# Kernel tuning notes

Hardware: AMD Instinct MI355X
Metric: run time of the kernel (lower is better)

Reference implementation:

```python
import jax, jax.numpy as jnp
import numpy as np

N, E, IN, H, C, ED = 100000, 1600000, 128, 4, 32, 16
HC = H * C
NEG_SLOPE = 0.2
EPS = 1e-5


def setup_inputs() -> dict:
    key = jax.random.key(0)
    ks = jax.random.split(key, 12)
    x = jax.random.normal(ks[0], (N, IN), jnp.float32)
    edge_index = jax.random.randint(ks[1], (2, E), 0, N, dtype=jnp.int32)
    edge_attr = jax.random.normal(ks[2], (E, ED), jnp.float32)
    s_in = 1.0 / np.sqrt(IN)
    s_ed = 1.0 / np.sqrt(ED)
    s_c = 1.0 / np.sqrt(C)
    Wl = jax.random.normal(ks[3], (IN, HC), jnp.float32) * s_in
    bl = jnp.zeros((HC,), jnp.float32)
    Wr = jax.random.normal(ks[4], (IN, HC), jnp.float32) * s_in
    br = jnp.zeros((HC,), jnp.float32)
    We = jax.random.normal(ks[5], (ED, HC), jnp.float32) * s_ed
    att = jax.random.normal(ks[6], (H, C), jnp.float32) * s_c
    bias = jnp.zeros((HC,), jnp.float32)
    ln_weight = jnp.ones((HC,), jnp.float32)
    ln_bias = jnp.zeros((HC,), jnp.float32)
    return {"x": x, "edge_index": edge_index, "edge_attr": edge_attr,
            "Wl": Wl, "bl": bl, "Wr": Wr, "br": br, "We": We,
            "att": att, "bias": bias, "ln_weight": ln_weight, "ln_bias": ln_bias}


def gatv2_block(x, src, dst, edge_attr, Wl, bl, Wr, br, We, att, bias, ln_weight, ln_bias):
    n = x.shape[0]
    xl = (x @ Wl + bl).reshape(n, H, C)  # source-side transform
    xr = (x @ Wr + br).reshape(n, H, C)  # target-side transform
    # add_self_loops with fill_value='mean': self-loop edge_attr = mean of
    # incoming edge_attr per node (0 for isolated nodes)
    ea_sum = jax.ops.segment_sum(edge_attr, dst, num_segments=n)
    cnt = jax.ops.segment_sum(jnp.ones((edge_attr.shape[0],), edge_attr.dtype), dst, num_segments=n)
    self_attr = ea_sum / jnp.maximum(cnt, 1.0)[:, None]
    loop = jnp.arange(n, dtype=src.dtype)
    src_a = jnp.concatenate([src, loop])
    dst_a = jnp.concatenate([dst, loop])
    ea_a = jnp.concatenate([edge_attr, self_attr], axis=0)
    e_emb = (ea_a @ We).reshape(-1, H, C)
    # GATv2 attention: a^T LeakyReLU(xl_j + xr_i + e)
    m = xl[src_a] + xr[dst_a] + e_emb            # [Etot, H, C]
    m = jax.nn.leaky_relu(m, NEG_SLOPE)
    alpha = jnp.einsum('ehc,hc->eh', m, att)     # [Etot, H]
    amax = jax.ops.segment_max(alpha, dst_a, num_segments=n)
    alpha = jnp.exp(alpha - amax[dst_a])
    denom = jax.ops.segment_sum(alpha, dst_a, num_segments=n)
    alpha = alpha / denom[dst_a]
    out = jax.ops.segment_sum(xl[src_a] * alpha[:, :, None], dst_a, num_segments=n)
    h = out.reshape(n, HC) + bias
    # residual (in_dim == H*C so no projection), PyG graph-mode LayerNorm
    z = x + h
    mu = jnp.mean(z)
    var = jnp.mean((z - mu) ** 2)
    z = (z - mu) / jnp.sqrt(var + EPS)
    z = z * ln_weight + ln_bias
    return jax.nn.relu(z)  # dropout = identity in eval


def reference(x, edge_index, edge_attr, Wl, bl, Wr, br, We, att, bias, ln_weight, ln_bias):
    src, dst = edge_index[0], edge_index[1]
    return gatv2_block(x, src, dst, edge_attr, Wl, bl, Wr, br, We, att, bias, ln_weight, ln_bias)
```

## Files before the change

### kernel.cpp

```cpp
#include <hip/hip_runtime.h>
#include <hip/hip_bf16.h>

static constexpr float NEG_SLOPE = 0.2f;
static constexpr float LN_EPS = 1e-5f;

typedef float v2f __attribute__((ext_vector_type(2)));
typedef __attribute__((ext_vector_type(8))) short bf16x8;
typedef __attribute__((ext_vector_type(4))) float f32x4;

__device__ __forceinline__ unsigned f2b(float f) {
  unsigned u = __float_as_uint(f);
  return (u + 0x7fffu + ((u >> 16) & 1u)) >> 16;
}
__device__ __forceinline__ v2f b2f2(ushort2 u) {
  v2f r;
  r.x = __uint_as_float((unsigned)u.x << 16);
  r.y = __uint_as_float((unsigned)u.y << 16);
  return r;
}
__device__ __forceinline__ float sbl(unsigned w) {
  return __uint_as_float(w << 16);
}
__device__ __forceinline__ float sbh(unsigned w) {
  return __uint_as_float(w & 0xFFFF0000u);
}

__device__ __forceinline__ float head_sum16(float x) {
  float t;
  t = __int_as_float(__builtin_amdgcn_update_dpp(
      0, __float_as_int(x), 0xB1, 0xF, 0xF, true));
  x += t;
  t = __int_as_float(__builtin_amdgcn_update_dpp(
      0, __float_as_int(x), 0x4E, 0xF, 0xF, true));
  x += t;
  t = __int_as_float(__builtin_amdgcn_update_dpp(
      0, __float_as_int(x), 0x124, 0xF, 0xF, true));
  x += t;
  t = __int_as_float(__builtin_amdgcn_update_dpp(
      0, __float_as_int(x), 0x128, 0xF, 0xF, true));
  x += t;
  return x;
}

__global__ __launch_bounds__(256) void k_packB(
    const float* __restrict__ Wl, const float* __restrict__ Wr,
    const float* __restrict__ bl, const float* __restrict__ br,
    ushort* __restrict__ Bpack, float* __restrict__ bcat)
{
  int tid = blockIdx.x * 256 + threadIdx.x;
  int l = tid & 63, s = (tid >> 6) & 3, t = tid >> 8;
  int col = t * 16 + (l & 15);
  int kb = s * 32 + (l >> 4) * 8;
  const float* __restrict__ W = (col < 128) ? Wl : Wr;
  int c = col & 127;
  unsigned p[4];
#pragma unroll
  for (int i = 0; i < 4; ++i) {
    unsigned lo = f2b(W[(size_t)(kb + 2 * i) * 128 + c]);
    unsigned hi = f2b(W[(size_t)(kb + 2 * i + 1) * 128 + c]);
    p[i] = lo | (hi << 16);
  }
  *(uint4*)(Bpack + (size_t)tid * 8) = make_uint4(p[0], p[1], p[2], p[3]);
  if (tid < 256) bcat[tid] = (tid < 128) ? bl[tid] : br[tid - 128];
}

__global__ __launch_bounds__(256) void k_gemm_mfma(
    const float* __restrict__ x, const ushort* __restrict__ Bpack,
    const float* __restrict__ bcat, ushort* __restrict__ xl,
    float* __restrict__ outz, int n)
{
  const int lane = threadIdx.x & 63;
  const int w = threadIdx.x >> 6;
  const int row0 = blockIdx.x * 64 + w * 16;
  const int rowA = min(row0 + (lane & 15), n - 1);
  const int kgrp = lane >> 4;

  f32x4 acc[16];
#pragma unroll
  for (int t = 0; t < 16; ++t) acc[t] = (f32x4){0.f, 0.f, 0.f, 0.f};

#pragma unroll
  for (int s = 0; s < 4; ++s) {
    const float4* ap =
        (const float4*)(x + (size_t)rowA * 128 + s * 32 + kgrp * 8);
    float4 a0 = ap[0], a1 = ap[1];
    bf16x8 a;
    a[0] = (short)f2b(a0.x); a[1] = (short)f2b(a0.y);
    a[2] = (short)f2b(a0.z); a[3] = (short)f2b(a0.w);
    a[4] = (short)f2b(a1.x); a[5] = (short)f2b(a1.y);
    a[6] = (short)f2b(a1.z); a[7] = (short)f2b(a1.w);
#pragma unroll
    for (int t = 0; t < 16; ++t) {
      bf16x8 b =
          *(const bf16x8*)(Bpack + (((size_t)t * 4 + s) * 64 + lane) * 8);
      acc[t] = __builtin_amdgcn_mfma_f32_16x16x32_bf16(a, b, acc[t], 0, 0, 0);
    }
  }

  const int colg = lane & 15;
  const int rbase = row0 + (lane >> 4) * 4;
#pragma unroll
  for (int t = 0; t < 16; ++t) {
    const int col = t * 16 + colg;
    const float bia = bcat[col];
    if (col < 128) {
#pragma unroll
      for (int r = 0; r < 4; ++r) {
        const int R = rbase + r;
        if (R < n) xl[(size_t)R * 128 + col] = (ushort)f2b(acc[t][r] + bia);
      }
    } else {
      const int c = col - 128;
#pragma unroll
      for (int r = 0; r < 4; ++r) {
        const int R = rbase + r;
        if (R < n) outz[(size_t)R * 128 + c] = acc[t][r] + bia;
      }
    }
  }
}

__global__ __launch_bounds__(256) void k_count(const int* __restrict__ dst,
                                               int* __restrict__ deg, int E)
{
  int e = blockIdx.x * 256 + threadIdx.x;
  if (e < E) atomicAdd(&deg[dst[e]], 1);
}

__global__ __launch_bounds__(256) void k_scan1(const int* __restrict__ deg,
                                               int* __restrict__ bsum, int n)
{
  int i = blockIdx.x * 256 + threadIdx.x;
  int v = (i < n) ? deg[i] : 0;
#pragma unroll
  for (int o = 32; o > 0; o >>= 1) v += __shfl_down(v, o);
  __shared__ int ls[4];
  if ((threadIdx.x & 63) == 0) ls[threadIdx.x >> 6] = v;
  __syncthreads();
  if (threadIdx.x == 0) bsum[blockIdx.x] = ls[0] + ls[1] + ls[2] + ls[3];
}

__global__ __launch_bounds__(512) void k_scan2(int* __restrict__ bsum, int nb)
{
  __shared__ int s[512];
  int t = threadIdx.x;
  int v = (t < nb) ? bsum[t] : 0;
  s[t] = v;
  __syncthreads();
  for (int o = 1; o < 512; o <<= 1) {
    int u = (t >= o) ? s[t - o] : 0;
    __syncthreads();
    s[t] += u;
    __syncthreads();
  }
  if (t < nb) bsum[t] = s[t] - v;
}

__global__ __launch_bounds__(256) void k_scan3(const int* __restrict__ deg,
                                               const int* __restrict__ bsum,
                                               int* __restrict__ offs, int n)
{
  __shared__ int s[256];
  int b = blockIdx.x, t = threadIdx.x, i = b * 256 + t;
  int v = (i < n) ? deg[i] : 0;
  s[t] = v;
  __syncthreads();
  for (int o = 1; o < 256; o <<= 1) {
    int u = (t >= o) ? s[t - o] : 0;
    __syncthreads();
    s[t] += u;
    __syncthreads();
  }
  if (i < n) offs[i] = bsum[b] + s[t] - v;
}

__global__ __launch_bounds__(256) void k_fill(
    const int* __restrict__ src, const int* __restrict__ dst,
    const int* __restrict__ offs, int* __restrict__ cursor,
    const float4* __restrict__ ea4, int* __restrict__ csr_src,
    ushort* __restrict__ csr_ea, int E)
{
  int e = blockIdx.x * 256 + threadIdx.x;
  if (e >= E) return;
  int d = dst[e];
  int pos = offs[d] + atomicAdd(&cursor[d], 1);
  csr_src[pos] = src[e];
  float4 r0 = ea4[(size_t)e * 4 + 0], r1 = ea4[(size_t)e * 4 + 1];
  float4 r2 = ea4[(size_t)e * 4 + 2], r3 = ea4[(size_t)e * 4 + 3];
  uint4* o4 = (uint4*)(csr_ea + (size_t)pos * 16);
  o4[0] = make_uint4(f2b(r0.x) | (f2b(r0.y) << 16), f2b(r0.z) | (f2b(r0.w) << 16),
                     f2b(r1.x) | (f2b(r1.y) << 16), f2b(r1.z) | (f2b(r1.w) << 16));
  o4[1] = make_uint4(f2b(r2.x) | (f2b(r2.y) << 16), f2b(r2.z) | (f2b(r2.w) << 16),
                     f2b(r3.x) | (f2b(r3.y) << 16), f2b(r3.z) | (f2b(r3.w) << 16));
}

__global__ __launch_bounds__(256) void k_fused(
    const int* __restrict__ csr_src, const ushort* __restrict__ csr_ea,
    const int* __restrict__ offs, const int* __restrict__ deg,
    const ushort* __restrict__ xl, const float* __restrict__ We,
    const float* __restrict__ att, const float* __restrict__ x,
    const float* __restrict__ bias, float* __restrict__ outz,
    double* __restrict__ red, int N)
{
  const int lane = threadIdx.x & 63;
  const int gw =
      __builtin_amdgcn_readfirstlane(blockIdx.x * 4 + (threadIdx.x >> 6));
  const int nw = gridDim.x * 4;
  const v2f* __restrict__ We2 = (const v2f*)We;
  const v2f* __restrict__ X2 = (const v2f*)x;
  v2f* __restrict__ Z2 = (v2f*)outz;

  v2f we[16];
#pragma unroll
  for (int k = 0; k < 16; ++k) we[k] = We2[k * 64 + lane];
  const v2f a2 = ((const v2f*)att)[lane];
  const v2f b2 = ((const v2f*)bias)[lane];

  float sred = 0.f, s2red = 0.f;

  for (int node = gw; node < N; node += nw) {
    const int beg = offs[node];
    const int len = deg[node];
    const v2f xrv = Z2[(size_t)node * 64 + lane];
    const v2f xvSelf =
        b2f2(*(const ushort2*)(xl + (size_t)node * 128 + 2 * lane));

    float dA = 0.f, dB = 0.f;
    v2f aA = {0.f, 0.f}, aB = {0.f, 0.f};
    v2f embsum = {0.f, 0.f};

    auto edgeU = [&](v2f xv, uint4 lo, uint4 hi, float& den, v2f& acc) {
      v2f emb = sbl(lo.x) * we[0];
      emb += sbh(lo.x) * we[1];
      emb += sbl(lo.y) * we[2];
      emb += sbh(lo.y) * we[3];
      emb += sbl(lo.z) * we[4];
      emb += sbh(lo.z) * we[5];
      emb += sbl(lo.w) * we[6];
      emb += sbh(lo.w) * we[7];
      emb += sbl(hi.x) * we[8];
      emb += sbh(hi.x) * we[9];
      emb += sbl(hi.y) * we[10];
      emb += sbh(hi.y) * we[11];
      emb += sbl(hi.z) * we[12];
      emb += sbh(hi.z) * we[13];
      emb += sbl(hi.w) * we[14];
      emb += sbh(hi.w) * we[15];
      embsum += emb;
      v2f mm = xv + xrv + emb;
      v2f ml;
      ml.x = fmaxf(mm.x, NEG_SLOPE * mm.x);
      ml.y = fmaxf(mm.y, NEG_SLOPE * mm.y);
      const float part = head_sum16(fmaf(ml.y, a2.y, ml.x * a2.x));
      const float p = __expf(part);
      den += p;
      acc += xv * p;
    };

    const int nB = len >> 1;
    const int nA = len - nB;
    const int bB = beg + nA;

    uint4 eAlo = {0, 0, 0, 0}, eAhi = {0, 0, 0, 0};
    uint4 eBlo = {0, 0, 0, 0}, eBhi = {0, 0, 0, 0};
    v2f xvA = {0.f, 0.f}, xvB = {0.f, 0.f};
    int sA1 = 0, sB1 = 0;

    if (len > 0) {
      const uint4* pa = (const uint4*)(csr_ea + (size_t)beg * 16);
      eAlo = pa[0];
      eAhi = pa[1];
      const int sA0 = csr_src[beg];
      xvA = b2f2(*(const ushort2*)(xl + (size_t)sA0 * 128 + 2 * lane));
      sA1 = csr_src[beg + 1];
    }
    if (nB > 0) {
      const uint4* pb = (const uint4*)(csr_ea + (size_t)bB * 16);
      eBlo = pb[0];
      eBhi = pb[1];
      const int sB0 = csr_src[bB];
      xvB = b2f2(*(const ushort2*)(xl + (size_t)sB0 * 128 + 2 * lane));
      sB1 = csr_src[bB + 1];
    }

    for (int i = 0; i < nB; ++i) {
      const uint4* pa = (const uint4*)(csr_ea + (size_t)(beg + i + 1) * 16);
      const uint4* pb = (const uint4*)(csr_ea + (size_t)(bB + i + 1) * 16);
      const uint4 nAlo = pa[0], nAhi = pa[1];
      const uint4 nBlo = pb[0], nBhi = pb[1];
      const v2f xvA1 =
          b2f2(*(const ushort2*)(xl + (size_t)sA1 * 128 + 2 * lane));
      const v2f xvB1 =
          b2f2(*(const ushort2*)(xl + (size_t)sB1 * 128 + 2 * lane));
      const int sA2 = csr_src[beg + i + 2];
      const int sB2 = csr_src[bB + i + 2];
      edgeU(xvA, eAlo, eAhi, dA, aA);
      edgeU(xvB, eBlo, eBhi, dB, aB);
      eAlo = nAlo; eAhi = nAhi; eBlo = nBlo; eBhi = nBhi;
      xvA = xvA1; xvB = xvB1;
      sA1 = sA2; sB1 = sB2;
    }
    if (nA > nB) {
      edgeU(xvA, eAlo, eAhi, dA, aA);
    }

    {
      const float inv = (len > 0) ? 1.f / (float)len : 0.f;
      const v2f embS = embsum * inv;
      v2f mm = xvSelf + xrv + embS;
      v2f ml;
      ml.x = fmaxf(mm.x, NEG_SLOPE * mm.x);
      ml.y = fmaxf(mm.y, NEG_SLOPE * mm.y);
      const float part = head_sum16(fmaf(ml.y, a2.y, ml.x * a2.x));
      const float p = __expf(part);
      dA += p;
      aA += xvSelf * p;
    }

    const float den = dA + dB;
    const float invden = 1.f / den;
    const float o0 = (aA.x + aB.x) * invden;
    const float o1 = (aA.y + aB.y) * invden;

    const v2f xvn = X2[(size_t)node * 64 + lane];
    const float v0 = xvn.x + o0 + b2.x;
    const float v1 = xvn.y + o1 + b2.y;
    Z2[(size_t)node * 64 + lane] = (v2f){v0, v1};
    sred += v0 + v1;
    s2red += v0 * v0 + v1 * v1;
  }

#pragma unroll
  for (int o = 32; o > 0; o >>= 1) {
    sred += __shfl_down(sred, o);
    s2red += __shfl_down(s2red, o);
  }
  __shared__ double ls[4], ls2[4];
  const int w = threadIdx.x >> 6;
  if ((threadIdx.x & 63) == 0) {
    ls[w] = (double)sred;
    ls2[w] = (double)s2red;
  }
  __syncthreads();
  if (threadIdx.x == 0) {
    unsafeAtomicAdd(red, ls[0] + ls[1] + ls[2] + ls[3]);
    unsafeAtomicAdd(red + 1, ls2[0] + ls2[1] + ls2[2] + ls2[3]);
  }
}

__global__ __launch_bounds__(256) void k_final(
    float* __restrict__ z, const double* __restrict__ red,
    const float* __restrict__ lnw, const float* __restrict__ lnb, int M4)
{
  int i = blockIdx.x * 256 + threadIdx.x;
  if (i >= M4) return;
  const double invM = 1.0 / ((double)M4 * 4.0);
  const double mu = red[0] * invM;
  const double var = red[1] * invM - mu * mu;
  const float sc = rsqrtf((float)var + LN_EPS);
  const float muf = (float)mu;
  const float4* W4 = (const float4*)lnw;
  const float4* L4 = (const float4*)lnb;
  float4* Z4 = (float4*)z;
  float4 zv = Z4[i], wv = W4[i & 31], lv = L4[i & 31];
  float4 o;
  o.x = fmaxf((zv.x - muf) * sc * wv.x + lv.x, 0.f);
  o.y = fmaxf((zv.y - muf) * sc * wv.y + lv.y, 0.f);
  o.z = fmaxf((zv.z - muf) * sc * wv.z + lv.z, 0.f);
  o.w = fmaxf((zv.w - muf) * sc * wv.w + lv.w, 0.f);
  Z4[i] = o;
}

extern "C" void kernel_launch(void* const* d_in, const int* in_sizes, int n_in,
                              void* d_out, int out_size, void* d_ws,
                              size_t ws_size, hipStream_t stream)
{
  const float* x = (const float*)d_in[0];
  const int* ei = (const int*)d_in[1];
  const float* edge_attr = (const float*)d_in[2];
  const float* Wl = (const float*)d_in[3];
  const float* bl = (const float*)d_in[4];
  const float* Wr = (const float*)d_in[5];
  const float* br = (const float*)d_in[6];
  const float* We = (const float*)d_in[7];
  const float* att = (const float*)d_in[8];
  const float* bias = (const float*)d_in[9];
  const float* lnw = (const float*)d_in[10];
  const float* lnb = (const float*)d_in[11];
  float* out = (float*)d_out;

  const int N = in_sizes[0] / 128;
  const int E = in_sizes[1] / 2;
  const int M = N * 128;
  const int* srcp = ei;
  const int* dstp = ei + E;
  const int nb = (N + 255) / 256;

  ushort* xl = (ushort*)d_ws;
  int* deg = (int*)(xl + (size_t)M);
  int* cursor = deg + N;
  int* offs = cursor + N;
  int* bsum = offs + N;
  int* csr_src = bsum + ((nb + 7) & ~7);
  ushort* csr_ea =
      (ushort*)((((size_t)(csr_src + E + 8)) + 63) & ~(size_t)63);
  double* red = (double*)(
      (((size_t)(csr_ea + (size_t)E * 16 + 16)) + 127) & ~(size_t)127);
  ushort* Bpack = (ushort*)(red + 8);
  float* bcat = (float*)(Bpack + 4096 * 8);

  hipMemsetAsync(deg, 0, (size_t)N * 8, stream);
  hipMemsetAsync(csr_src + E, 0, 32, stream);
  hipMemsetAsync(red, 0, 16, stream);

  k_packB<<<16, 256, 0, stream>>>(Wl, Wr, bl, br, Bpack, bcat);
  k_gemm_mfma<<<(N + 63) / 64, 256, 0, stream>>>(x, Bpack, bcat, xl, out, N);
  k_count<<<(E + 255) / 256, 256, 0, stream>>>(dstp, deg, E);
  k_scan1<<<nb, 256, 0, stream>>>(deg, bsum, N);
  k_scan2<<<1, 512, 0, stream>>>(bsum, nb);
  k_scan3<<<nb, 256, 0, stream>>>(deg, bsum, offs, N);
  k_fill<<<(E + 255) / 256, 256, 0, stream>>>(srcp, dstp, offs, cursor,
                                              (const float4*)edge_attr,
                                              csr_src, csr_ea, E);
  k_fused<<<2048, 256, 0, stream>>>(csr_src, csr_ea, offs, deg, xl, We, att,
                                    x, bias, out, red, N);
  k_final<<<(M / 4 + 255) / 256, 256, 0, stream>>>(out, red, lnw, lnb, M / 4);
}
```

Measured before the change: 498.5 us.

## Deepen edge-attr prefetch to two edges, split emb FMA chain, fold memsets into packB

In the fused edge loop, edge attributes are now prefetched two iterations ahead instead of one, so more loads are in flight to hide memory latency. The serial 16-term embedding accumulation is split into four independent chains to shorten the dependency path. Two small memsets are moved into the k_packB kernel to cut API launch overhead, and the padding after csr_ea is enlarged to cover the deeper prefetch. The cost is higher register pressure from the extra buffered uint4 values, plus slightly different floating-point summation order.

Measured after the change: 499.6 us. About the same (+0.2%).

```diff
diff --git a/kernel.cpp b/kernel.cpp
--- a/kernel.cpp
+++ b/kernel.cpp
@@ -45,7 +45,8 @@
 __global__ __launch_bounds__(256) void k_packB(
     const float* __restrict__ Wl, const float* __restrict__ Wr,
     const float* __restrict__ bl, const float* __restrict__ br,
-    ushort* __restrict__ Bpack, float* __restrict__ bcat)
+    ushort* __restrict__ Bpack, float* __restrict__ bcat,
+    int* __restrict__ src_pad, double* __restrict__ red)
 {
   int tid = blockIdx.x * 256 + threadIdx.x;
   int l = tid & 63, s = (tid >> 6) & 3, t = tid >> 8;
@@ -62,6 +63,8 @@
   }
   *(uint4*)(Bpack + (size_t)tid * 8) = make_uint4(p[0], p[1], p[2], p[3]);
   if (tid < 256) bcat[tid] = (tid < 128) ? bl[tid] : br[tid - 128];
+  if (tid < 8) src_pad[tid] = 0;
+  if (tid < 2) red[tid] = 0.0;
 }
 
 __global__ __launch_bounds__(256) void k_gemm_mfma(
@@ -230,22 +233,23 @@
     v2f embsum = {0.f, 0.f};
 
     auto edgeU = [&](v2f xv, uint4 lo, uint4 hi, float& den, v2f& acc) {
-      v2f emb = sbl(lo.x) * we[0];
-      emb += sbh(lo.x) * we[1];
-      emb += sbl(lo.y) * we[2];
-      emb += sbh(lo.y) * we[3];
-      emb += sbl(lo.z) * we[4];
-      emb += sbh(lo.z) * we[5];
-      emb += sbl(lo.w) * we[6];
-      emb += sbh(lo.w) * we[7];
-      emb += sbl(hi.x) * we[8];
-      emb += sbh(hi.x) * we[9];
-      emb += sbl(hi.y) * we[10];
-      emb += sbh(hi.y) * we[11];
-      emb += sbl(hi.z) * we[12];
-      emb += sbh(hi.z) * we[13];
-      emb += sbl(hi.w) * we[14];
-      emb += sbh(hi.w) * we[15];
+      v2f e0 = sbl(lo.x) * we[0];
+      v2f e1 = sbh(lo.x) * we[1];
+      v2f e2 = sbl(lo.y) * we[2];
+      v2f e3 = sbh(lo.y) * we[3];
+      e0 += sbl(lo.z) * we[4];
+      e1 += sbh(lo.z) * we[5];
+      e2 += sbl(lo.w) * we[6];
+      e3 += sbh(lo.w) * we[7];
+      e0 += sbl(hi.x) * we[8];
+      e1 += sbh(hi.x) * we[9];
+      e2 += sbl(hi.y) * we[10];
+      e3 += sbh(hi.y) * we[11];
+      e0 += sbl(hi.z) * we[12];
+      e1 += sbh(hi.z) * we[13];
+      e2 += sbl(hi.w) * we[14];
+      e3 += sbh(hi.w) * we[15];
+      const v2f emb = (e0 + e1) + (e2 + e3);
       embsum += emb;
       v2f mm = xv + xrv + emb;
       v2f ml;
@@ -262,7 +266,9 @@
     const int bB = beg + nA;
 
     uint4 eAlo = {0, 0, 0, 0}, eAhi = {0, 0, 0, 0};
+    uint4 eA1lo = {0, 0, 0, 0}, eA1hi = {0, 0, 0, 0};
     uint4 eBlo = {0, 0, 0, 0}, eBhi = {0, 0, 0, 0};
+    uint4 eB1lo = {0, 0, 0, 0}, eB1hi = {0, 0, 0, 0};
     v2f xvA = {0.f, 0.f}, xvB = {0.f, 0.f};
     int sA1 = 0, sB1 = 0;
 
@@ -270,6 +276,9 @@
       const uint4* pa = (const uint4*)(csr_ea + (size_t)beg * 16);
       eAlo = pa[0];
       eAhi = pa[1];
+      const uint4* pa1 = (const uint4*)(csr_ea + (size_t)(beg + 1) * 16);
+      eA1lo = pa1[0];
+      eA1hi = pa1[1];
       const int sA0 = csr_src[beg];
       xvA = b2f2(*(const ushort2*)(xl + (size_t)sA0 * 128 + 2 * lane));
       sA1 = csr_src[beg + 1];
@@ -278,16 +287,19 @@
       const uint4* pb = (const uint4*)(csr_ea + (size_t)bB * 16);
       eBlo = pb[0];
       eBhi = pb[1];
+      const uint4* pb1 = (const uint4*)(csr_ea + (size_t)(bB + 1) * 16);
+      eB1lo = pb1[0];
+      eB1hi = pb1[1];
       const int sB0 = csr_src[bB];
       xvB = b2f2(*(const ushort2*)(xl + (size_t)sB0 * 128 + 2 * lane));
       sB1 = csr_src[bB + 1];
     }
 
     for (int i = 0; i < nB; ++i) {
-      const uint4* pa = (const uint4*)(csr_ea + (size_t)(beg + i + 1) * 16);
-      const uint4* pb = (const uint4*)(csr_ea + (size_t)(bB + i + 1) * 16);
-      const uint4 nAlo = pa[0], nAhi = pa[1];
-      const uint4 nBlo = pb[0], nBhi = pb[1];
+      const uint4* pa2 = (const uint4*)(csr_ea + (size_t)(beg + i + 2) * 16);
+      const uint4* pb2 = (const uint4*)(csr_ea + (size_t)(bB + i + 2) * 16);
+      const uint4 eA2lo = pa2[0], eA2hi = pa2[1];
+      const uint4 eB2lo = pb2[0], eB2hi = pb2[1];
       const v2f xvA1 =
           b2f2(*(const ushort2*)(xl + (size_t)sA1 * 128 + 2 * lane));
       const v2f xvB1 =
@@ -296,7 +308,8 @@
       const int sB2 = csr_src[bB + i + 2];
       edgeU(xvA, eAlo, eAhi, dA, aA);
       edgeU(xvB, eBlo, eBhi, dB, aB);
-      eAlo = nAlo; eAhi = nAhi; eBlo = nBlo; eBhi = nBhi;
+      eAlo = eA1lo; eAhi = eA1hi; eA1lo = eA2lo; eA1hi = eA2hi;
+      eBlo = eB1lo; eBhi = eB1hi; eB1lo = eB2lo; eB1hi = eB2hi;
       xvA = xvA1; xvB = xvB1;
       sA1 = sA2; sB1 = sB2;
     }
@@ -405,15 +418,14 @@
   ushort* csr_ea =
       (ushort*)((((size_t)(csr_src + E + 8)) + 63) & ~(size_t)63);
   double* red = (double*)(
-      (((size_t)(csr_ea + (size_t)E * 16 + 16)) + 127) & ~(size_t)127);
+      (((size_t)(csr_ea + (size_t)E * 16 + 64)) + 127) & ~(size_t)127);
   ushort* Bpack = (ushort*)(red + 8);
   float* bcat = (float*)(Bpack + 4096 * 8);
 
   hipMemsetAsync(deg, 0, (size_t)N * 8, stream);
-  hipMemsetAsync(csr_src + E, 0, 32, stream);
-  hipMemsetAsync(red, 0, 16, stream);
-
-  k_packB<<<16, 256, 0, stream>>>(Wl, Wr, bl, br, Bpack, bcat);
+
+  k_packB<<<16, 256, 0, stream>>>(Wl, Wr, bl, br, Bpack, bcat, csr_src + E,
+                                  red);
   k_gemm_mfma<<<(N + 63) / 64, 256, 0, stream>>>(x, Bpack, bcat, xl, out, N);
   k_count<<<(E + 255) / 256, 256, 0, stream>>>(dstp, deg, E);
   k_scan1<<<nb, 256, 0, stream>>>(deg, bsum, N);
```

## Store xl in fp32, fuse degree count into GEMM, fold memsets into packB

Applied to the files above, without the earlier changes.

Switches the xl intermediate from bf16 to fp32, which doubles its storage and the bytes of every per-edge gather in the fused kernel but removes the bf16 pack/unpack steps. The per-edge degree atomic count moves into the tail of the GEMM kernel as a grid-stride loop, and the small memsets for the CSR padding and reduction accumulators move into the packB kernel. Together these drop two memsets and one kernel launch, at the cost of heavier gather traffic in the main aggregation loop.

After: 491.7 us. No clear change (-1.4%).

```diff
diff --git a/kernel.cpp b/kernel.cpp
--- a/kernel.cpp
+++ b/kernel.cpp
@@ -11,12 +11,6 @@
 __device__ __forceinline__ unsigned f2b(float f) {
   unsigned u = __float_as_uint(f);
   return (u + 0x7fffu + ((u >> 16) & 1u)) >> 16;
-}
-__device__ __forceinline__ v2f b2f2(ushort2 u) {
-  v2f r;
-  r.x = __uint_as_float((unsigned)u.x << 16);
-  r.y = __uint_as_float((unsigned)u.y << 16);
-  return r;
 }
 __device__ __forceinline__ float sbl(unsigned w) {
   return __uint_as_float(w << 16);
@@ -45,7 +39,8 @@
 __global__ __launch_bounds__(256) void k_packB(
     const float* __restrict__ Wl, const float* __restrict__ Wr,
     const float* __restrict__ bl, const float* __restrict__ br,
-    ushort* __restrict__ Bpack, float* __restrict__ bcat)
+    ushort* __restrict__ Bpack, float* __restrict__ bcat,
+    int* __restrict__ src_pad, double* __restrict__ red)
 {
   int tid = blockIdx.x * 256 + threadIdx.x;
   int l = tid & 63, s = (tid >> 6) & 3, t = tid >> 8;
@@ -62,12 +57,15 @@
   }
   *(uint4*)(Bpack + (size_t)tid * 8) = make_uint4(p[0], p[1], p[2], p[3]);
   if (tid < 256) bcat[tid] = (tid < 128) ? bl[tid] : br[tid - 128];
+  if (tid < 8) src_pad[tid] = 0;
+  if (tid < 2) red[tid] = 0.0;
 }
 
 __global__ __launch_bounds__(256) void k_gemm_mfma(
     const float* __restrict__ x, const ushort* __restrict__ Bpack,
-    const float* __restrict__ bcat, ushort* __restrict__ xl,
-    float* __restrict__ outz, int n)
+    const float* __restrict__ bcat, float* __restrict__ xl,
+    float* __restrict__ outz, int n, const int* __restrict__ dst,
+    int* __restrict__ deg, int E)
 {
   const int lane = threadIdx.x & 63;
   const int w = threadIdx.x >> 6;
@@ -103,28 +101,17 @@
   for (int t = 0; t < 16; ++t) {
     const int col = t * 16 + colg;
     const float bia = bcat[col];
-    if (col < 128) {
-#pragma unroll
-      for (int r = 0; r < 4; ++r) {
-        const int R = rbase + r;
-        if (R < n) xl[(size_t)R * 128 + col] = (ushort)f2b(acc[t][r] + bia);
-      }
-    } else {
-      const int c = col - 128;
-#pragma unroll
-      for (int r = 0; r < 4; ++r) {
-        const int R = rbase + r;
-        if (R < n) outz[(size_t)R * 128 + c] = acc[t][r] + bia;
-      }
-    }
-  }
-}
-
-__global__ __launch_bounds__(256) void k_count(const int* __restrict__ dst,
-                                               int* __restrict__ deg, int E)
-{
-  int e = blockIdx.x * 256 + threadIdx.x;
-  if (e < E) atomicAdd(&deg[dst[e]], 1);
+    float* __restrict__ outp = (col < 128) ? xl : outz;
+    const int c = col & 127;
+#pragma unroll
+    for (int r = 0; r < 4; ++r) {
+      const int R = rbase + r;
+      if (R < n) outp[(size_t)R * 128 + c] = acc[t][r] + bia;
+    }
+  }
+
+  for (int e = blockIdx.x * 256 + threadIdx.x; e < E; e += gridDim.x * 256)
+    atomicAdd(&deg[dst[e]], 1);
 }
 
 __global__ __launch_bounds__(256) void k_scan1(const int* __restrict__ deg,
@@ -197,7 +184,7 @@
 __global__ __launch_bounds__(256) void k_fused(
     const int* __restrict__ csr_src, const ushort* __restrict__ csr_ea,
     const int* __restrict__ offs, const int* __restrict__ deg,
-    const ushort* __restrict__ xl, const float* __restrict__ We,
+    const float* __restrict__ xl, const float* __restrict__ We,
     const float* __restrict__ att, const float* __restrict__ x,
     const float* __restrict__ bias, float* __restrict__ outz,
     double* __restrict__ red, int N)
@@ -207,6 +194,7 @@
       __builtin_amdgcn_readfirstlane(blockIdx.x * 4 + (threadIdx.x >> 6));
   const int nw = gridDim.x * 4;
   const v2f* __restrict__ We2 = (const v2f*)We;
+  const v2f* __restrict__ Xl2 = (const v2f*)xl;
   const v2f* __restrict__ X2 = (const v2f*)x;
   v2f* __restrict__ Z2 = (v2f*)outz;
 
@@ -222,8 +210,7 @@
     const int beg = offs[node];
     const int len = deg[node];
     const v2f xrv = Z2[(size_t)node * 64 + lane];
-    const v2f xvSelf =
-        b2f2(*(const ushort2*)(xl + (size_t)node * 128 + 2 * lane));
+    const v2f xvSelf = Xl2[(size_t)node * 64 + lane];
 
     float dA = 0.f, dB = 0.f;
     v2f aA = {0.f, 0.f}, aB = {0.f, 0.f};
@@ -271,7 +258,7 @@
       eAlo = pa[0];
       eAhi = pa[1];
       const int sA0 = csr_src[beg];
-      xvA = b2f2(*(const ushort2*)(xl + (size_t)sA0 * 128 + 2 * lane));
+      xvA = Xl2[(size_t)sA0 * 64 + lane];
       sA1 = csr_src[beg + 1];
     }
     if (nB > 0) {
@@ -279,7 +266,7 @@
       eBlo = pb[0];
       eBhi = pb[1];
       const int sB0 = csr_src[bB];
-      xvB = b2f2(*(const ushort2*)(xl + (size_t)sB0 * 128 + 2 * lane));
+      xvB = Xl2[(size_t)sB0 * 64 + lane];
       sB1 = csr_src[bB + 1];
     }
 
@@ -288,10 +275,8 @@
       const uint4* pb = (const uint4*)(csr_ea + (size_t)(bB + i + 1) * 16);
       const uint4 nAlo = pa[0], nAhi = pa[1];
       const uint4 nBlo = pb[0], nBhi = pb[1];
-      const v2f xvA1 =
-          b2f2(*(const ushort2*)(xl + (size_t)sA1 * 128 + 2 * lane));
-      const v2f xvB1 =
-          b2f2(*(const ushort2*)(xl + (size_t)sB1 * 128 + 2 * lane));
+      const v2f xvA1 = Xl2[(size_t)sA1 * 64 + lane];
+      const v2f xvB1 = Xl2[(size_t)sB1 * 64 + lane];
       const int sA2 = csr_src[beg + i + 2];
       const int sB2 = csr_src[bB + i + 2];
       edgeU(xvA, eAlo, eAhi, dA, aA);
@@ -396,7 +381,7 @@
   const int* dstp = ei + E;
   const int nb = (N + 255) / 256;
 
-  ushort* xl = (ushort*)d_ws;
+  float* xl = (float*)d_ws;
   int* deg = (int*)(xl + (size_t)M);
   int* cursor = deg + N;
   int* offs = cursor + N;
@@ -405,17 +390,16 @@
   ushort* csr_ea =
       (ushort*)((((size_t)(csr_src + E + 8)) + 63) & ~(size_t)63);
   double* red = (double*)(
-      (((size_t)(csr_ea + (size_t)E * 16 + 16)) + 127) & ~(size_t)127);
+      (((size_t)(csr_ea + (size_t)E * 16 + 64)) + 127) & ~(size_t)127);
   ushort* Bpack = (ushort*)(red + 8);
   float* bcat = (float*)(Bpack + 4096 * 8);
 
   hipMemsetAsync(deg, 0, (size_t)N * 8, stream);
-  hipMemsetAsync(csr_src + E, 0, 32, stream);
-  hipMemsetAsync(red, 0, 16, stream);
-
-  k_packB<<<16, 256, 0, stream>>>(Wl, Wr, bl, br, Bpack, bcat);
-  k_gemm_mfma<<<(N + 63) / 64, 256, 0, stream>>>(x, Bpack, bcat, xl, out, N);
-  k_count<<<(E + 255) / 256, 256, 0, stream>>>(dstp, deg, E);
+
+  k_packB<<<16, 256, 0, stream>>>(Wl, Wr, bl, br, Bpack, bcat, csr_src + E,
+                                  red);
+  k_gemm_mfma<<<(N + 63) / 64, 256, 0, stream>>>(x, Bpack, bcat, xl, out, N,
+                                                 dstp, deg, E);
   k_scan1<<<nb, 256, 0, stream>>>(deg, bsum, N);
   k_scan2<<<1, 512, 0, stream>>>(bsum, nb);
   k_scan3<<<nb, 256, 0, stream>>>(deg, bsum, offs, N);
```

## Fuse memsets and degree count into existing kernels, replace three-pass scan with atomic allocation

Applied to the files above, without the earlier changes.

Moves the zeroing of degree/cursor arrays, padding and reduction buffers into the weight-packing kernel, and folds the per-edge degree count into the tail of the GEMM kernel. It also replaces the three-kernel prefix scan with a single kernel in which each block scans locally and reserves its base offset through an atomic counter. CSR segments are then no longer laid out in node order, which relies on consumers using offs/deg rather than contiguity. The aim is fewer launches and memsets, at the cost of nondeterministic segment placement and extra work added to the GEMM.

Measured after the change: 485.2 us, median of 2. 1.03x faster.

```diff
diff --git a/kernel.cpp b/kernel.cpp
--- a/kernel.cpp
+++ b/kernel.cpp
@@ -45,7 +45,9 @@
 __global__ __launch_bounds__(256) void k_packB(
     const float* __restrict__ Wl, const float* __restrict__ Wr,
     const float* __restrict__ bl, const float* __restrict__ br,
-    ushort* __restrict__ Bpack, float* __restrict__ bcat)
+    ushort* __restrict__ Bpack, float* __restrict__ bcat,
+    int* __restrict__ degcur, int N2, int* __restrict__ tot,
+    int* __restrict__ src_pad, double* __restrict__ red)
 {
   int tid = blockIdx.x * 256 + threadIdx.x;
   int l = tid & 63, s = (tid >> 6) & 3, t = tid >> 8;
@@ -62,12 +64,17 @@
   }
   *(uint4*)(Bpack + (size_t)tid * 8) = make_uint4(p[0], p[1], p[2], p[3]);
   if (tid < 256) bcat[tid] = (tid < 128) ? bl[tid] : br[tid - 128];
+  if (tid < 8) src_pad[tid] = 0;
+  if (tid < 2) red[tid] = 0.0;
+  if (tid == 0) *tot = 0;
+  for (int i = tid; i < N2; i += 4096) degcur[i] = 0;
 }
 
 __global__ __launch_bounds__(256) void k_gemm_mfma(
     const float* __restrict__ x, const ushort* __restrict__ Bpack,
     const float* __restrict__ bcat, ushort* __restrict__ xl,
-    float* __restrict__ outz, int n)
+    float* __restrict__ outz, int n, const int* __restrict__ dst,
+    int* __restrict__ deg, int E)
 {
   const int lane = threadIdx.x & 63;
   const int w = threadIdx.x >> 6;
@@ -118,51 +125,19 @@
       }
     }
   }
-}
-
-__global__ __launch_bounds__(256) void k_count(const int* __restrict__ dst,
-                                               int* __restrict__ deg, int E)
-{
-  int e = blockIdx.x * 256 + threadIdx.x;
-  if (e < E) atomicAdd(&deg[dst[e]], 1);
-}
-
-__global__ __launch_bounds__(256) void k_scan1(const int* __restrict__ deg,
-                                               int* __restrict__ bsum, int n)
-{
-  int i = blockIdx.x * 256 + threadIdx.x;
-  int v = (i < n) ? deg[i] : 0;
-#pragma unroll
-  for (int o = 32; o > 0; o >>= 1) v += __shfl_down(v, o);
-  __shared__ int ls[4];
-  if ((threadIdx.x & 63) == 0) ls[threadIdx.x >> 6] = v;
-  __syncthreads();
-  if (threadIdx.x == 0) bsum[blockIdx.x] = ls[0] + ls[1] + ls[2] + ls[3];
-}
-
-__global__ __launch_bounds__(512) void k_scan2(int* __restrict__ bsum, int nb)
-{
-  __shared__ int s[512];
-  int t = threadIdx.x;
-  int v = (t < nb) ? bsum[t] : 0;
-  s[t] = v;
-  __syncthreads();
-  for (int o = 1; o < 512; o <<= 1) {
-    int u = (t >= o) ? s[t - o] : 0;
-    __syncthreads();
-    s[t] += u;
-    __syncthreads();
-  }
-  if (t < nb) bsum[t] = s[t] - v;
-}
-
-__global__ __launch_bounds__(256) void k_scan3(const int* __restrict__ deg,
-                                               const int* __restrict__ bsum,
-                                               int* __restrict__ offs, int n)
+
+  for (int e = blockIdx.x * 256 + threadIdx.x; e < E; e += gridDim.x * 256)
+    atomicAdd(&deg[dst[e]], 1);
+}
+
+__global__ __launch_bounds__(256) void k_allocscan(
+    const int* __restrict__ deg, int* __restrict__ offs, int* __restrict__ tot,
+    int n)
 {
   __shared__ int s[256];
-  int b = blockIdx.x, t = threadIdx.x, i = b * 256 + t;
-  int v = (i < n) ? deg[i] : 0;
+  __shared__ int base;
+  const int b = blockIdx.x, t = threadIdx.x, i = b * 256 + t;
+  const int v = (i < n) ? deg[i] : 0;
   s[t] = v;
   __syncthreads();
   for (int o = 1; o < 256; o <<= 1) {
@@ -171,7 +146,9 @@
     s[t] += u;
     __syncthreads();
   }
-  if (i < n) offs[i] = bsum[b] + s[t] - v;
+  if (t == 255) base = atomicAdd(tot, s[255]);
+  __syncthreads();
+  if (i < n) offs[i] = base + s[t] - v;
 }
 
 __global__ __launch_bounds__(256) void k_fill(
@@ -400,25 +377,20 @@
   int* deg = (int*)(xl + (size_t)M);
   int* cursor = deg + N;
   int* offs = cursor + N;
-  int* bsum = offs + N;
-  int* csr_src = bsum + ((nb + 7) & ~7);
+  int* tot = offs + N;
+  int* csr_src = tot + 8;
   ushort* csr_ea =
       (ushort*)((((size_t)(csr_src + E + 8)) + 63) & ~(size_t)63);
   double* red = (double*)(
-      (((size_t)(csr_ea + (size_t)E * 16 + 16)) + 127) & ~(size_t)127);
+      (((size_t)(csr_ea + (size_t)E * 16 + 64)) + 127) & ~(size_t)127);
   ushort* Bpack = (ushort*)(red + 8);
   float* bcat = (float*)(Bpack + 4096 * 8);
 
-  hipMemsetAsync(deg, 0, (size_t)N * 8, stream);
-  hipMemsetAsync(csr_src + E, 0, 32, stream);
-  hipMemsetAsync(red, 0, 16, stream);
-
-  k_packB<<<16, 256, 0, stream>>>(Wl, Wr, bl, br, Bpack, bcat);
-  k_gemm_mfma<<<(N + 63) / 64, 256, 0, stream>>>(x, Bpack, bcat, xl, out, N);
-  k_count<<<(E + 255) / 256, 256, 0, stream>>>(dstp, deg, E);
-  k_scan1<<<nb, 256, 0, stream>>>(deg, bsum, N);
-  k_scan2<<<1, 512, 0, stream>>>(bsum, nb);
-  k_scan3<<<nb, 256, 0, stream>>>(deg, bsum, offs, N);
+  k_packB<<<16, 256, 0, stream>>>(Wl, Wr, bl, br, Bpack, bcat, deg, 2 * N,
+                                  tot, csr_src + E, red);
+  k_gemm_mfma<<<(N + 63) / 64, 256, 0, stream>>>(x, Bpack, bcat, xl, out, N,
+                                                 dstp, deg, E);
+  k_allocscan<<<nb, 256, 0, stream>>>(deg, offs, tot, N);
   k_fill<<<(E + 255) / 256, 256, 0, stream>>>(srcp, dstp, offs, cursor,
                                               (const float4*)edge_attr,
                                               csr_src, csr_ea, E);
```
